# Optimization experiments

Measured on AMD Instinct MI355X. Metric: run time of the kernel, lower is better.

The kernel has to match this reference:

```python
import jax, jax.numpy as jnp
import numpy as np

N, L, H, V = 8192, 512, 64, 50000
NUM_PARENT = 1024


def setup_inputs() -> dict:
    key = jax.random.key(0)
    ks = jax.random.split(key, 12)
    def mat(k, shape):
        return 0.1 * jax.random.normal(k, shape, dtype=jnp.float32)
    return {
        "x_word": jax.random.normal(ks[0], (N, L), dtype=jnp.float32),
        "x_index": jax.random.randint(ks[1], (N, L), 0, V),
        "tree": jax.random.randint(ks[2], (N, 2), 0, N),
        "num_parent": NUM_PARENT,
        "embedding": mat(ks[3], (V, H)),
        "W_z": mat(ks[4], (H, H)),
        "U_z": mat(ks[5], (H, H)),
        "b_z": jnp.zeros((H,), dtype=jnp.float32),
        "W_r": mat(ks[6], (H, H)),
        "U_r": mat(ks[7], (H, H)),
        "b_r": jnp.zeros((H,), dtype=jnp.float32),
        "W_h": mat(ks[8], (H, H)),
        "U_h": mat(ks[9], (H, H)),
        "b_h": jnp.zeros((H,), dtype=jnp.float32),
    }


def _hard_sigmoid(x):
    # torch double-threshold trick == clip(0.2*x + 0.5, 0, 1)
    return jnp.clip(0.2 * x + 0.5, 0.0, 1.0)


def reference(x_word, x_index, tree, num_parent, embedding,
              W_z, U_z, b_z, W_r, U_r, b_r, W_h, U_h, b_h):
    n_nodes = x_word.shape[0]
    hdim = embedding.shape[1]

    def step(node_h, xs):
        word, idx, info = xs  # word: [L] f32, idx: [L] int, info: [2] int
        parent_h = node_h[info[0]]                 # [H]
        child_xe = embedding[idx].T @ word         # [H] weighted embedding sum
        z = _hard_sigmoid(W_z @ child_xe + U_z @ parent_h + b_z)
        r = _hard_sigmoid(W_r @ child_xe + U_r @ parent_h + b_r)
        c = jnp.tanh(W_h @ child_xe + U_h @ (parent_h * r) + b_h)
        h = z * parent_h + (1.0 - z) * c           # [H]
        return node_h.at[info[1]].set(h), h

    node_h0 = jnp.zeros((n_nodes, hdim), dtype=x_word.dtype)
    # original loops i in range(len(x_word) - 1)
    _, child_hs = jax.lax.scan(step, node_h0,
                               (x_word[:-1], x_index[:-1], tree[:-1]))
    # output = max over child_hs[num_parent-1:]
    return jnp.max(child_hs[num_parent - 1:], axis=0)
```

## Files before the change

### kernel.cpp

```cpp
#include <hip/hip_runtime.h>
#include <math.h>

#define NODES  8192
#define STEPS  8191
#define LW     512
#define H      64
#define VOCAB  50000
#define RWAVES 512

typedef __attribute__((ext_vector_type(2))) float f32x2;

__global__ void ws_too_small_kernel(float* __restrict__ out) {
    if (threadIdx.x < H) out[threadIdx.x] = -12345.0f;
}

__global__ __launch_bounds__(256)
void cvt_emb(const float* __restrict__ emb, unsigned int* __restrict__ embq) {
    int i = blockIdx.x * 256 + threadIdx.x;
    float4 v = reinterpret_cast<const float4*>(emb)[i];
    int w = 0;
    w = __builtin_amdgcn_cvt_pk_fp8_f32(v.x, v.y, w, false);
    w = __builtin_amdgcn_cvt_pk_fp8_f32(v.z, v.w, w, true);
    embq[i] = (unsigned int)w;
}

__global__ __launch_bounds__(1024)
void build_schedule(const int* __restrict__ tree, int* __restrict__ writers_g,
                    int* __restrict__ pred_g, int* __restrict__ lstart_g,
                    int* __restrict__ order_g) {
    __shared__ int s_off[NODES + 8];
    __shared__ int wsum[16];
    int tid  = threadIdx.x;
    int lane = tid & 63;
    int wv   = tid >> 6;

    for (int i = tid; i < NODES + 8; i += 1024) s_off[i] = 0;
    __syncthreads();
    for (int j = tid; j < STEPS; j += 1024)
        atomicAdd(&s_off[tree[2 * j + 1]], 1);
    __syncthreads();

    {
        int base = tid * 8;
        int v[8], run = 0;
        #pragma unroll
        for (int e = 0; e < 8; ++e) { v[e] = run; run += s_off[base + e]; }
        int x = run;
        #pragma unroll
        for (int d = 1; d < 64; d <<= 1) {
            int y = __shfl_up(x, d, 64);
            if (lane >= d) x += y;
        }
        if (lane == 63) wsum[wv] = x;
        __syncthreads();
        if (wv == 0) {
            int s = (lane < 16) ? wsum[lane] : 0;
            #pragma unroll
            for (int d = 1; d < 16; d <<= 1) {
                int y = __shfl_up(s, d, 64);
                if (lane >= d) s += y;
            }
            if (lane < 16) wsum[lane] = s;
        }
        __syncthreads();
        int wbase = (wv > 0) ? wsum[wv - 1] : 0;
        int tbase = wbase + x - run;
        #pragma unroll
        for (int e = 0; e < 8; ++e) s_off[base + e] = tbase + v[e];
    }
    __syncthreads();

    for (int j = tid; j < STEPS; j += 1024) {
        int v = tree[2 * j + 1];
        int pos = atomicAdd(&s_off[v], 1);
        writers_g[pos] = j;
    }
    __syncthreads();

    int pr[8];
    #pragma unroll
    for (int e = 0; e < 8; ++e) {
        int i = tid + e * 1024;
        int best = -1;
        if (i < STEPS) {
            int v  = tree[2 * i];
            int t1 = s_off[v];
            int t0 = (v > 0) ? s_off[v - 1] : 0;
            for (int t = t0; t < t1; ++t) {
                int j = writers_g[t];
                if (j < i && j > best) best = j;
            }
            pred_g[i] = best;
        }
        pr[e] = best;
    }
    __syncthreads();

    short* jmp = (short*)s_off;
    short* dep = (short*)s_off + NODES;
    #pragma unroll
    for (int e = 0; e < 8; ++e) {
        int i = tid + e * 1024;
        jmp[i] = (short)pr[e];
        dep[i] = (pr[e] >= 0) ? 1 : 0;
    }
    __syncthreads();

    for (int r = 0; r < 13; ++r) {
        short nd[8], nj[8];
        #pragma unroll
        for (int e = 0; e < 8; ++e) {
            int i = tid + e * 1024;
            int j = jmp[i];
            if (j >= 0) { nd[e] = (short)(dep[i] + dep[j]); nj[e] = jmp[j]; }
            else        { nd[e] = dep[i];                   nj[e] = -1;     }
        }
        __syncthreads();
        #pragma unroll
        for (int e = 0; e < 8; ++e) {
            int i = tid + e * 1024;
            dep[i] = nd[e];
            jmp[i] = nj[e];
        }
        __syncthreads();
    }

    int d8[8];
    #pragma unroll
    for (int e = 0; e < 8; ++e) d8[e] = dep[tid + e * 1024];
    __syncthreads();

    int* lcnt = s_off;
    for (int i = tid; i < NODES; i += 1024) lcnt[i] = 0;
    __syncthreads();
    #pragma unroll
    for (int e = 0; e < 8; ++e) {
        int i = tid + e * 1024;
        if (i < STEPS) atomicAdd(&lcnt[d8[e]], 1);
    }
    __syncthreads();
    {
        int base = tid * 8;
        int v[8], run = 0;
        #pragma unroll
        for (int e = 0; e < 8; ++e) { v[e] = run; run += lcnt[base + e]; }
        int x = run;
        #pragma unroll
        for (int d = 1; d < 64; d <<= 1) {
            int y = __shfl_up(x, d, 64);
            if (lane >= d) x += y;
        }
        if (lane == 63) wsum[wv] = x;
        __syncthreads();
        if (wv == 0) {
            int s = (lane < 16) ? wsum[lane] : 0;
            #pragma unroll
            for (int d = 1; d < 16; d <<= 1) {
                int y = __shfl_up(s, d, 64);
                if (lane >= d) s += y;
            }
            if (lane < 16) wsum[lane] = s;
        }
        __syncthreads();
        int wbase = (wv > 0) ? wsum[wv - 1] : 0;
        int tbase = wbase + x - run;
        #pragma unroll
        for (int e = 0; e < 8; ++e) lstart_g[base + e] = tbase + v[e];
        if (tid == 1023) lstart_g[8192] = tbase + run;
    }
    __threadfence_block();
    __syncthreads();

    for (int i = tid; i < NODES; i += 1024) lcnt[i] = 0;
    __syncthreads();
    #pragma unroll
    for (int e = 0; e < 8; ++e) {
        int i = tid + e * 1024;
        if (i < STEPS) {
            int d = d8[e];
            int pos = atomicAdd(&lcnt[d], 1);
            order_g[lstart_g[d] + pos] = i;
        }
    }
}

__global__ __launch_bounds__(256)
void gather_project(const float* __restrict__ xw, const int* __restrict__ xi,
                    const unsigned int* __restrict__ embq,
                    const float* __restrict__ Wz, const float* __restrict__ Wr,
                    const float* __restrict__ Wh,
                    const float* __restrict__ bz, const float* __restrict__ br,
                    const float* __restrict__ bh,
                    const int* __restrict__ pred,
                    float* __restrict__ A, float* __restrict__ child_h,
                    int* __restrict__ done) {
    int i    = blockIdx.x;
    int tid  = threadIdx.x;
    int wave = tid >> 6;
    int lane = tid & 63;
    int g16  = lane >> 2;
    int q4   = lane & 3;

    __shared__ float s_w[LW];
    __shared__ int   s_idx[LW];
    __shared__ float part[4][64];
    __shared__ float xe[64];

    {
        float2 w2 = reinterpret_cast<const float2*>(xw + (size_t)i * LW)[tid];
        int2   i2 = reinterpret_cast<const int2*>(xi + (size_t)i * LW)[tid];
        s_w[2 * tid]     = w2.x;
        s_w[2 * tid + 1] = w2.y;
        s_idx[2 * tid]     = i2.x;
        s_idx[2 * tid + 1] = i2.y;
    }
    __syncthreads();

    const uint4* E = reinterpret_cast<const uint4*>(embq);
    int base_l = wave * 128 + g16;

    float acc[16];
    #pragma unroll
    for (int c = 0; c < 16; ++c) acc[c] = 0.f;

    uint4 q[8];
    float wgt[8];
    #pragma unroll
    for (int u = 0; u < 8; ++u) {
        int l   = base_l + u * 16;
        int idx = s_idx[l];
        wgt[u]  = s_w[l];
        q[u]    = E[(size_t)idx * 4 + q4];
    }
    #pragma unroll
    for (int u = 0; u < 8; ++u) {
        float w = wgt[u];
        unsigned int uw[4] = {q[u].x, q[u].y, q[u].z, q[u].w};
        #pragma unroll
        for (int d = 0; d < 4; ++d) {
            f32x2 lo = __builtin_amdgcn_cvt_pk_f32_fp8((int)uw[d], false);
            f32x2 hi = __builtin_amdgcn_cvt_pk_f32_fp8((int)uw[d], true);
            acc[4 * d + 0] = fmaf(w, lo.x, acc[4 * d + 0]);
            acc[4 * d + 1] = fmaf(w, lo.y, acc[4 * d + 1]);
            acc[4 * d + 2] = fmaf(w, hi.x, acc[4 * d + 2]);
            acc[4 * d + 3] = fmaf(w, hi.y, acc[4 * d + 3]);
        }
    }
    #pragma unroll
    for (int c = 0; c < 16; ++c) {
        acc[c] += __shfl_xor(acc[c], 4,  64);
        acc[c] += __shfl_xor(acc[c], 8,  64);
        acc[c] += __shfl_xor(acc[c], 16, 64);
        acc[c] += __shfl_xor(acc[c], 32, 64);
    }
    if (lane < 4) {
        #pragma unroll
        for (int c = 0; c < 16; ++c) part[wave][lane * 16 + c] = acc[c];
    }
    __syncthreads();
    if (tid < 64) xe[tid] = part[0][tid] + part[1][tid] + part[2][tid] + part[3][tid];
    __syncthreads();

    float s = 0.f;
    if (tid < 192) {
        int o = tid & 63;
        const float* W = (tid < 64) ? Wz : (tid < 128 ? Wr : Wh);
        const float* b = (tid < 64) ? bz : (tid < 128 ? br : bh);
        s = b[o];
        #pragma unroll
        for (int j = 0; j < H; j += 4) {
            float4 w4 = *reinterpret_cast<const float4*>(W + (size_t)o * H + j);
            s = fmaf(w4.x, xe[j],     s);
            s = fmaf(w4.y, xe[j + 1], s);
            s = fmaf(w4.z, xe[j + 2], s);
            s = fmaf(w4.w, xe[j + 3], s);
        }
    }
    bool isroot = (pred[i] < 0);
    if (tid == 0) done[i] = isroot ? 1 : 0;
    if (tid < 64)                part[0][tid]       = s;
    if (tid >= 128 && tid < 192) part[1][tid - 128] = s;
    __syncthreads();
    if (isroot) {
        if (tid < 64) {
            float z = fminf(fmaxf(0.2f * part[0][tid] + 0.5f, 0.f), 1.f);
            float c = tanhf(part[1][tid]);
            child_h[(size_t)i * H + tid] = (1.f - z) * c;
        }
    } else {
        if (tid < 192) A[(size_t)i * 192 + tid] = s;
    }
}

__global__ __launch_bounds__(256)
void recurrence(const int* __restrict__ lstart, const int* __restrict__ order,
                const float* __restrict__ A, const int* __restrict__ pred,
                const float* __restrict__ Uz, const float* __restrict__ Ur,
                const float* __restrict__ Uh, float* __restrict__ child_h,
                int* __restrict__ done) {
    int gw   = (blockIdx.x * blockDim.x + threadIdx.x) >> 6;
    int lane = threadIdx.x & 63;
    int t0   = lstart[1];
    if (t0 + gw >= STEPS) return;

    float uz[H], ur[H], uh[H];
    #pragma unroll
    for (int j = 0; j < H; j += 4) {
        float4 a4 = *reinterpret_cast<const float4*>(Uz + (size_t)lane * H + j);
        uz[j] = a4.x; uz[j+1] = a4.y; uz[j+2] = a4.z; uz[j+3] = a4.w;
        float4 b4 = *reinterpret_cast<const float4*>(Ur + (size_t)lane * H + j);
        ur[j] = b4.x; ur[j+1] = b4.y; ur[j+2] = b4.z; ur[j+3] = b4.w;
        float4 c4 = *reinterpret_cast<const float4*>(Uh + (size_t)lane * H + j);
        uh[j] = c4.x; uh[j+1] = c4.y; uh[j+2] = c4.z; uh[j+3] = c4.w;
    }

    for (int t = t0 + gw; t < STEPS; t += RWAVES) {
        int i = order[t];
        int p = pred[i];
        const float* Ai = A + (size_t)i * 192;
        float az = Ai[lane];
        float ar = Ai[64 + lane];
        float ah = Ai[128 + lane];

        int guard = 0;
        while (__hip_atomic_load(done + p, __ATOMIC_RELAXED,
                                 __HIP_MEMORY_SCOPE_AGENT) == 0) {
            __builtin_amdgcn_s_sleep(1);
            if (++guard > (1 << 22)) break;
        }
        __threadfence();

        float ph = child_h[(size_t)p * H + lane];
        #pragma unroll
        for (int j = 0; j < H; ++j) {
            float s = __shfl(ph, j, 64);
            az = fmaf(uz[j], s, az);
            ar = fmaf(ur[j], s, ar);
        }
        float z = fminf(fmaxf(0.2f * az + 0.5f, 0.f), 1.f);
        float r = fminf(fmaxf(0.2f * ar + 0.5f, 0.f), 1.f);
        float phr = ph * r;
        #pragma unroll
        for (int j = 0; j < H; ++j) {
            float s = __shfl(phr, j, 64);
            ah = fmaf(uh[j], s, ah);
        }
        float c = tanhf(ah);
        child_h[(size_t)i * H + lane] = z * ph + (1.f - z) * c;
        __threadfence();
        if (lane == 0)
            __hip_atomic_store(done + i, 1, __ATOMIC_RELAXED,
                               __HIP_MEMORY_SCOPE_AGENT);
    }
}

__global__ __launch_bounds__(256)
void reduce_partial(const float* __restrict__ child_h,
                    const int* __restrict__ np_ptr,
                    float* __restrict__ partial) {
    int b   = blockIdx.x;
    int tid = threadIdx.x;
    int h   = tid & 63;
    int grp = tid >> 6;
    int np    = *np_ptr;
    int start = np - 1;
    int total = STEPS - start;
    int per   = (total + gridDim.x - 1) / gridDim.x;
    int r0 = start + b * per;
    int r1 = r0 + per; if (r1 > STEPS) r1 = STEPS;
    float m = -INFINITY;
    for (int row = r0 + grp; row < r1; row += 4)
        m = fmaxf(m, child_h[(size_t)row * H + h]);
    __shared__ float sm[4][64];
    sm[grp][h] = m;
    __syncthreads();
    if (tid < 64)
        partial[b * 64 + tid] = fmaxf(fmaxf(sm[0][tid], sm[1][tid]),
                                      fmaxf(sm[2][tid], sm[3][tid]));
}

__global__ void reduce_final(const float* __restrict__ partial,
                             float* __restrict__ out, int nb) {
    int h = threadIdx.x;
    float m = -INFINITY;
    for (int b = 0; b < nb; ++b) m = fmaxf(m, partial[b * 64 + h]);
    out[h] = m;
}

extern "C" void kernel_launch(void* const* d_in, const int* in_sizes, int n_in,
                              void* d_out, int out_size, void* d_ws, size_t ws_size,
                              hipStream_t stream) {
    const float* xw   = (const float*)d_in[0];
    const int*   xi   = (const int*)  d_in[1];
    const int*   tree = (const int*)  d_in[2];
    const int*   np   = (const int*)  d_in[3];
    const float* emb  = (const float*)d_in[4];
    const float* Wz   = (const float*)d_in[5];
    const float* Uz   = (const float*)d_in[6];
    const float* bz   = (const float*)d_in[7];
    const float* Wr   = (const float*)d_in[8];
    const float* Ur   = (const float*)d_in[9];
    const float* br   = (const float*)d_in[10];
    const float* Wh   = (const float*)d_in[11];
    const float* Uh   = (const float*)d_in[12];
    const float* bh   = (const float*)d_in[13];

    size_t bA   = (size_t)STEPS * 192 * 4;
    size_t bCH  = (size_t)STEPS * H   * 4;
    size_t bEH  = (size_t)VOCAB * H   * 1;
    size_t bInt = (size_t)(8192 * 4 + 8256) * 4;
    size_t bPar = 56 * 64 * 4 + 256;
    size_t need = bA + bCH + bEH + bInt + bPar;
    if (ws_size < need) {
        ws_too_small_kernel<<<1, 64, 0, stream>>>((float*)d_out);
        return;
    }

    char* base = (char*)d_ws;
    float*          A       = (float*)base;                 base += bA;
    float*          child_h = (float*)base;                 base += bCH;
    unsigned int*   embq    = (unsigned int*)base;          base += bEH;
    int*            pred    = (int*)base;
    int*            writers = pred    + 8192;
    int*            order   = writers + 8192;
    int*            done    = order   + 8192;
    int*            lstart  = done    + 8192;
    float*          partial = (float*)(lstart + 8256);

    cvt_emb        <<<3125, 256, 0, stream>>>(emb, embq);

    build_schedule <<<1,  1024, 0, stream>>>(tree, writers, pred, lstart, order);

    gather_project <<<STEPS, 256, 0, stream>>>(xw, xi, embq, Wz, Wr, Wh,
                                               bz, br, bh, pred, A, child_h,
                                               done);

    recurrence     <<<128, 256, 0, stream>>>(lstart, order, A, pred,
                                             Uz, Ur, Uh, child_h, done);

    reduce_partial <<<56,  256, 0, stream>>>(child_h, np, partial);
    reduce_final   <<<1,    64, 0, stream>>>(partial, (float*)d_out, 56);
}
```

Baseline: 344.9 us.

## Replace spin-wait dataflow recurrence with level-synchronous launches and single-block tail

The atomic done-flag spin-wait recurrence is replaced by per-level kernel launches for the first few tree levels, followed by a single 1024-thread block that walks the remaining levels with __syncthreads barriers. Gather_project now handles 8 nodes per block and double-buffers the next node's word and index rows in shared memory. cvt_emb becomes a grid-stride loop over fewer blocks. This removes the global atomics, fences and polling, but the deep tail levels now run inside one workgroup and reload the U matrices for every node.

```diff
diff --git a/kernel.cpp b/kernel.cpp
--- a/kernel.cpp
+++ b/kernel.cpp
@@ -6,7 +6,8 @@
 #define LW     512
 #define H      64
 #define VOCAB  50000
-#define RWAVES 512
+#define SWEEPK 4
+#define GNODES 8
 
 typedef __attribute__((ext_vector_type(2))) float f32x2;
 
@@ -16,12 +17,14 @@
 
 __global__ __launch_bounds__(256)
 void cvt_emb(const float* __restrict__ emb, unsigned int* __restrict__ embq) {
-    int i = blockIdx.x * 256 + threadIdx.x;
-    float4 v = reinterpret_cast<const float4*>(emb)[i];
-    int w = 0;
-    w = __builtin_amdgcn_cvt_pk_fp8_f32(v.x, v.y, w, false);
-    w = __builtin_amdgcn_cvt_pk_fp8_f32(v.z, v.w, w, true);
-    embq[i] = (unsigned int)w;
+    const int total = VOCAB * H / 4;
+    for (int i = blockIdx.x * 256 + threadIdx.x; i < total; i += 256 * 256) {
+        float4 v = reinterpret_cast<const float4*>(emb)[i];
+        int w = 0;
+        w = __builtin_amdgcn_cvt_pk_fp8_f32(v.x, v.y, w, false);
+        w = __builtin_amdgcn_cvt_pk_fp8_f32(v.z, v.w, w, true);
+        embq[i] = (unsigned int)w;
+    }
 }
 
 __global__ __launch_bounds__(1024)
@@ -192,116 +195,170 @@
                     const float* __restrict__ bz, const float* __restrict__ br,
                     const float* __restrict__ bh,
                     const int* __restrict__ pred,
-                    float* __restrict__ A, float* __restrict__ child_h,
-                    int* __restrict__ done) {
-    int i    = blockIdx.x;
+                    float* __restrict__ A, float* __restrict__ child_h) {
     int tid  = threadIdx.x;
     int wave = tid >> 6;
     int lane = tid & 63;
     int g16  = lane >> 2;
     int q4   = lane & 3;
 
-    __shared__ float s_w[LW];
-    __shared__ int   s_idx[LW];
+    __shared__ float s_w[2][LW];
+    __shared__ int   s_idx[2][LW];
     __shared__ float part[4][64];
     __shared__ float xe[64];
 
-    {
-        float2 w2 = reinterpret_cast<const float2*>(xw + (size_t)i * LW)[tid];
-        int2   i2 = reinterpret_cast<const int2*>(xi + (size_t)i * LW)[tid];
-        s_w[2 * tid]     = w2.x;
-        s_w[2 * tid + 1] = w2.y;
-        s_idx[2 * tid]     = i2.x;
-        s_idx[2 * tid + 1] = i2.y;
-    }
-    __syncthreads();
+    int base   = blockIdx.x * GNODES;
+    int nlocal = STEPS - base;
+    if (nlocal <= 0) return;
+    if (nlocal > GNODES) nlocal = GNODES;
 
     const uint4* E = reinterpret_cast<const uint4*>(embq);
     int base_l = wave * 128 + g16;
 
-    float acc[16];
-    #pragma unroll
-    for (int c = 0; c < 16; ++c) acc[c] = 0.f;
-
-    uint4 q[8];
-    float wgt[8];
-    #pragma unroll
-    for (int u = 0; u < 8; ++u) {
-        int l   = base_l + u * 16;
-        int idx = s_idx[l];
-        wgt[u]  = s_w[l];
-        q[u]    = E[(size_t)idx * 4 + q4];
-    }
-    #pragma unroll
-    for (int u = 0; u < 8; ++u) {
-        float w = wgt[u];
-        unsigned int uw[4] = {q[u].x, q[u].y, q[u].z, q[u].w};
-        #pragma unroll
-        for (int d = 0; d < 4; ++d) {
-            f32x2 lo = __builtin_amdgcn_cvt_pk_f32_fp8((int)uw[d], false);
-            f32x2 hi = __builtin_amdgcn_cvt_pk_f32_fp8((int)uw[d], true);
-            acc[4 * d + 0] = fmaf(w, lo.x, acc[4 * d + 0]);
-            acc[4 * d + 1] = fmaf(w, lo.y, acc[4 * d + 1]);
-            acc[4 * d + 2] = fmaf(w, hi.x, acc[4 * d + 2]);
-            acc[4 * d + 3] = fmaf(w, hi.y, acc[4 * d + 3]);
-        }
-    }
-    #pragma unroll
-    for (int c = 0; c < 16; ++c) {
-        acc[c] += __shfl_xor(acc[c], 4,  64);
-        acc[c] += __shfl_xor(acc[c], 8,  64);
-        acc[c] += __shfl_xor(acc[c], 16, 64);
-        acc[c] += __shfl_xor(acc[c], 32, 64);
-    }
-    if (lane < 4) {
-        #pragma unroll
-        for (int c = 0; c < 16; ++c) part[wave][lane * 16 + c] = acc[c];
-    }
-    __syncthreads();
-    if (tid < 64) xe[tid] = part[0][tid] + part[1][tid] + part[2][tid] + part[3][tid];
-    __syncthreads();
-
-    float s = 0.f;
-    if (tid < 192) {
-        int o = tid & 63;
-        const float* W = (tid < 64) ? Wz : (tid < 128 ? Wr : Wh);
-        const float* b = (tid < 64) ? bz : (tid < 128 ? br : bh);
-        s = b[o];
-        #pragma unroll
-        for (int j = 0; j < H; j += 4) {
-            float4 w4 = *reinterpret_cast<const float4*>(W + (size_t)o * H + j);
-            s = fmaf(w4.x, xe[j],     s);
-            s = fmaf(w4.y, xe[j + 1], s);
-            s = fmaf(w4.z, xe[j + 2], s);
-            s = fmaf(w4.w, xe[j + 3], s);
-        }
-    }
-    bool isroot = (pred[i] < 0);
-    if (tid == 0) done[i] = isroot ? 1 : 0;
-    if (tid < 64)                part[0][tid]       = s;
-    if (tid >= 128 && tid < 192) part[1][tid - 128] = s;
-    __syncthreads();
-    if (isroot) {
-        if (tid < 64) {
-            float z = fminf(fmaxf(0.2f * part[0][tid] + 0.5f, 0.f), 1.f);
-            float c = tanhf(part[1][tid]);
-            child_h[(size_t)i * H + tid] = (1.f - z) * c;
-        }
-    } else {
-        if (tid < 192) A[(size_t)i * 192 + tid] = s;
-    }
+    {
+        float2 w2 = reinterpret_cast<const float2*>(xw + (size_t)base * LW)[tid];
+        int2   i2 = reinterpret_cast<const int2*>(xi + (size_t)base * LW)[tid];
+        s_w[0][2 * tid]     = w2.x;
+        s_w[0][2 * tid + 1] = w2.y;
+        s_idx[0][2 * tid]     = i2.x;
+        s_idx[0][2 * tid + 1] = i2.y;
+    }
+    __syncthreads();
+
+    int cur = 0;
+    for (int n = 0; n < nlocal; ++n) {
+        int node = base + n;
+
+        float2 pw; int2 pi;
+        bool havenext = (n + 1 < nlocal);
+        if (havenext) {
+            pw = reinterpret_cast<const float2*>(xw + (size_t)(node + 1) * LW)[tid];
+            pi = reinterpret_cast<const int2*>(xi + (size_t)(node + 1) * LW)[tid];
+        }
+
+        float acc[16];
+        #pragma unroll
+        for (int c = 0; c < 16; ++c) acc[c] = 0.f;
+
+        uint4 q[8];
+        float wgt[8];
+        #pragma unroll
+        for (int u = 0; u < 8; ++u) {
+            int l   = base_l + u * 16;
+            int idx = s_idx[cur][l];
+            wgt[u]  = s_w[cur][l];
+            q[u]    = E[(size_t)idx * 4 + q4];
+        }
+        #pragma unroll
+        for (int u = 0; u < 8; ++u) {
+            float w = wgt[u];
+            unsigned int uw[4] = {q[u].x, q[u].y, q[u].z, q[u].w};
+            #pragma unroll
+            for (int d = 0; d < 4; ++d) {
+                f32x2 lo = __builtin_amdgcn_cvt_pk_f32_fp8((int)uw[d], false);
+                f32x2 hi = __builtin_amdgcn_cvt_pk_f32_fp8((int)uw[d], true);
+                acc[4 * d + 0] = fmaf(w, lo.x, acc[4 * d + 0]);
+                acc[4 * d + 1] = fmaf(w, lo.y, acc[4 * d + 1]);
+                acc[4 * d + 2] = fmaf(w, hi.x, acc[4 * d + 2]);
+                acc[4 * d + 3] = fmaf(w, hi.y, acc[4 * d + 3]);
+            }
+        }
+        #pragma unroll
+        for (int c = 0; c < 16; ++c) {
+            acc[c] += __shfl_xor(acc[c], 4,  64);
+            acc[c] += __shfl_xor(acc[c], 8,  64);
+            acc[c] += __shfl_xor(acc[c], 16, 64);
+            acc[c] += __shfl_xor(acc[c], 32, 64);
+        }
+        if (lane < 4) {
+            #pragma unroll
+            for (int c = 0; c < 16; ++c) part[wave][lane * 16 + c] = acc[c];
+        }
+        __syncthreads();
+        if (tid < 64)
+            xe[tid] = part[0][tid] + part[1][tid] + part[2][tid] + part[3][tid];
+        __syncthreads();
+
+        float s = 0.f;
+        if (tid < 192) {
+            int o = tid & 63;
+            const float* W = (tid < 64) ? Wz : (tid < 128 ? Wr : Wh);
+            const float* b = (tid < 64) ? bz : (tid < 128 ? br : bh);
+            s = b[o];
+            #pragma unroll
+            for (int j = 0; j < H; j += 4) {
+                float4 w4 = *reinterpret_cast<const float4*>(W + (size_t)o * H + j);
+                s = fmaf(w4.x, xe[j],     s);
+                s = fmaf(w4.y, xe[j + 1], s);
+                s = fmaf(w4.z, xe[j + 2], s);
+                s = fmaf(w4.w, xe[j + 3], s);
+            }
+        }
+        bool isroot = (pred[node] < 0);
+        if (tid < 64)                part[0][tid]       = s;
+        if (tid >= 128 && tid < 192) part[1][tid - 128] = s;
+        __syncthreads();
+        if (isroot) {
+            if (tid < 64) {
+                float z = fminf(fmaxf(0.2f * part[0][tid] + 0.5f, 0.f), 1.f);
+                float c = tanhf(part[1][tid]);
+                child_h[(size_t)node * H + tid] = (1.f - z) * c;
+            }
+        } else {
+            if (tid < 192) A[(size_t)node * 192 + tid] = s;
+        }
+
+        if (havenext) {
+            int nxt = cur ^ 1;
+            s_w[nxt][2 * tid]     = pw.x;
+            s_w[nxt][2 * tid + 1] = pw.y;
+            s_idx[nxt][2 * tid]     = pi.x;
+            s_idx[nxt][2 * tid + 1] = pi.y;
+            __syncthreads();
+            cur = nxt;
+        }
+    }
+}
+
+__device__ __forceinline__ void gru_core(
+        int i, int lane, const float* __restrict__ A,
+        const int* __restrict__ pred,
+        const float* uz, const float* ur, const float* uh,
+        float* __restrict__ child_h) {
+    int p = pred[i];
+    float ph = (p >= 0) ? child_h[(size_t)p * H + lane] : 0.f;
+    const float* Ai = A + (size_t)i * 192;
+    float az = Ai[lane];
+    float ar = Ai[64 + lane];
+    float ah = Ai[128 + lane];
+
+    #pragma unroll
+    for (int j = 0; j < H; ++j) {
+        float s = __shfl(ph, j, 64);
+        az = fmaf(uz[j], s, az);
+        ar = fmaf(ur[j], s, ar);
+    }
+    float z = fminf(fmaxf(0.2f * az + 0.5f, 0.f), 1.f);
+    float r = fminf(fmaxf(0.2f * ar + 0.5f, 0.f), 1.f);
+    float phr = ph * r;
+    #pragma unroll
+    for (int j = 0; j < H; ++j) {
+        float s = __shfl(phr, j, 64);
+        ah = fmaf(uh[j], s, ah);
+    }
+    float c = tanhf(ah);
+    child_h[(size_t)i * H + lane] = z * ph + (1.f - z) * c;
 }
 
 __global__ __launch_bounds__(256)
-void recurrence(const int* __restrict__ lstart, const int* __restrict__ order,
-                const float* __restrict__ A, const int* __restrict__ pred,
-                const float* __restrict__ Uz, const float* __restrict__ Ur,
-                const float* __restrict__ Uh, float* __restrict__ child_h,
-                int* __restrict__ done) {
-    int gw   = (blockIdx.x * blockDim.x + threadIdx.x) >> 6;
+void sweep_lvl(int k, const int* __restrict__ lstart, const int* __restrict__ order,
+               const float* __restrict__ A, const int* __restrict__ pred,
+               const float* __restrict__ Uz, const float* __restrict__ Ur,
+               const float* __restrict__ Uh, float* __restrict__ child_h) {
+    int s0 = lstart[k], s1 = lstart[k + 1];
+    int wave = (blockIdx.x * blockDim.x + threadIdx.x) >> 6;
     int lane = threadIdx.x & 63;
-    int t0   = lstart[1];
-    if (t0 + gw >= STEPS) return;
+    if (s0 + wave >= s1) return;
 
     float uz[H], ur[H], uh[H];
     #pragma unroll
@@ -313,44 +370,35 @@
         float4 c4 = *reinterpret_cast<const float4*>(Uh + (size_t)lane * H + j);
         uh[j] = c4.x; uh[j+1] = c4.y; uh[j+2] = c4.z; uh[j+3] = c4.w;
     }
-
-    for (int t = t0 + gw; t < STEPS; t += RWAVES) {
-        int i = order[t];
-        int p = pred[i];
-        const float* Ai = A + (size_t)i * 192;
-        float az = Ai[lane];
-        float ar = Ai[64 + lane];
-        float ah = Ai[128 + lane];
-
-        int guard = 0;
-        while (__hip_atomic_load(done + p, __ATOMIC_RELAXED,
-                                 __HIP_MEMORY_SCOPE_AGENT) == 0) {
-            __builtin_amdgcn_s_sleep(1);
-            if (++guard > (1 << 22)) break;
-        }
-        __threadfence();
-
-        float ph = child_h[(size_t)p * H + lane];
-        #pragma unroll
-        for (int j = 0; j < H; ++j) {
-            float s = __shfl(ph, j, 64);
-            az = fmaf(uz[j], s, az);
-            ar = fmaf(ur[j], s, ar);
-        }
-        float z = fminf(fmaxf(0.2f * az + 0.5f, 0.f), 1.f);
-        float r = fminf(fmaxf(0.2f * ar + 0.5f, 0.f), 1.f);
-        float phr = ph * r;
-        #pragma unroll
-        for (int j = 0; j < H; ++j) {
-            float s = __shfl(phr, j, 64);
-            ah = fmaf(uh[j], s, ah);
-        }
-        float c = tanhf(ah);
-        child_h[(size_t)i * H + lane] = z * ph + (1.f - z) * c;
-        __threadfence();
-        if (lane == 0)
-            __hip_atomic_store(done + i, 1, __ATOMIC_RELAXED,
-                               __HIP_MEMORY_SCOPE_AGENT);
+    for (int t = s0 + wave; t < s1; t += 512)
+        gru_core(order[t], lane, A, pred, uz, ur, uh, child_h);
+}
+
+__global__ __launch_bounds__(1024)
+void tail_block(const int* __restrict__ lstart, const int* __restrict__ order,
+                const float* __restrict__ A, const int* __restrict__ pred,
+                const float* __restrict__ Uz, const float* __restrict__ Ur,
+                const float* __restrict__ Uh, float* __restrict__ child_h) {
+    int wave = threadIdx.x >> 6;
+    int lane = threadIdx.x & 63;
+    for (int k = SWEEPK; k < NODES; ++k) {
+        int s0 = lstart[k];
+        if (s0 >= STEPS) break;
+        int s1 = lstart[k + 1];
+        for (int t = s0 + wave; t < s1; t += 16) {
+            float uz[H], ur[H], uh[H];
+            #pragma unroll
+            for (int j = 0; j < H; j += 4) {
+                float4 a4 = *reinterpret_cast<const float4*>(Uz + (size_t)lane * H + j);
+                uz[j] = a4.x; uz[j+1] = a4.y; uz[j+2] = a4.z; uz[j+3] = a4.w;
+                float4 b4 = *reinterpret_cast<const float4*>(Ur + (size_t)lane * H + j);
+                ur[j] = b4.x; ur[j+1] = b4.y; ur[j+2] = b4.z; ur[j+3] = b4.w;
+                float4 c4 = *reinterpret_cast<const float4*>(Uh + (size_t)lane * H + j);
+                uh[j] = c4.x; uh[j+1] = c4.y; uh[j+2] = c4.z; uh[j+3] = c4.w;
+            }
+            gru_core(order[t], lane, A, pred, uz, ur, uh, child_h);
+        }
+        __syncthreads();
     }
 }
 
@@ -408,7 +456,7 @@
     size_t bA   = (size_t)STEPS * 192 * 4;
     size_t bCH  = (size_t)STEPS * H   * 4;
     size_t bEH  = (size_t)VOCAB * H   * 1;
-    size_t bInt = (size_t)(8192 * 4 + 8256) * 4;
+    size_t bInt = (size_t)(8192 * 3 + 8256) * 4;
     size_t bPar = 56 * 64 * 4 + 256;
     size_t need = bA + bCH + bEH + bInt + bPar;
     if (ws_size < need) {
@@ -423,20 +471,21 @@
     int*            pred    = (int*)base;
     int*            writers = pred    + 8192;
     int*            order   = writers + 8192;
-    int*            done    = order   + 8192;
-    int*            lstart  = done    + 8192;
+    int*            lstart  = order   + 8192;
     float*          partial = (float*)(lstart + 8256);
 
-    cvt_emb        <<<3125, 256, 0, stream>>>(emb, embq);
+    cvt_emb        <<<256, 256, 0, stream>>>(emb, embq);
 
     build_schedule <<<1,  1024, 0, stream>>>(tree, writers, pred, lstart, order);
 
-    gather_project <<<STEPS, 256, 0, stream>>>(xw, xi, embq, Wz, Wr, Wh,
-                                               bz, br, bh, pred, A, child_h,
-                                               done);
-
-    recurrence     <<<128, 256, 0, stream>>>(lstart, order, A, pred,
-                                             Uz, Ur, Uh, child_h, done);
+    gather_project <<<(STEPS + GNODES - 1) / GNODES, 256, 0, stream>>>(
+                       xw, xi, embq, Wz, Wr, Wh, bz, br, bh, pred, A, child_h);
+
+    for (int k = 1; k < SWEEPK; ++k)
+        sweep_lvl  <<<128, 256, 0, stream>>>(k, lstart, order, A, pred,
+                                             Uz, Ur, Uh, child_h);
+    tail_block     <<<1, 1024, 0, stream>>>(lstart, order, A, pred,
+                                            Uz, Ur, Uh, child_h);
 
     reduce_partial <<<56,  256, 0, stream>>>(child_h, np, partial);
     reduce_final   <<<1,    64, 0, stream>>>(partial, (float*)d_out, 56);
```

New measurement: 420.9 us. 22.0% more time.
